# Performance work log

Measured on AMD Instinct MI355X. Metric: run time of the kernel, lower is better.

Reference implementation:

```python
import jax, jax.numpy as jnp
import numpy as np

NUM_VOCAB = 50000
EMBED_DIM = 128
SENT_SIZE = 50
MAX_HOPS = 3
BATCH = 128
MEM_SIZE = 200


def position_encoding(sentence_size, embedding_dim):
    # vectorized version of the original double loop
    i = np.arange(1, embedding_dim + 1, dtype=np.float32)[:, None]  # [D,1]
    j = np.arange(1, sentence_size + 1, dtype=np.float32)[None, :]  # [1,S]
    enc = (i - (embedding_dim + 1) / 2.0) * (j - (sentence_size + 1) / 2.0)
    enc = 1.0 + 4.0 * enc / embedding_dim / sentence_size
    enc[:, -1] = 1.0
    return np.transpose(enc).astype(np.float32)  # [S,D]


def setup_inputs() -> dict:
    key = jax.random.key(0)
    k1, k2, k3, k4, k5 = jax.random.split(key, 5)
    story = jax.random.randint(k1, (BATCH, MEM_SIZE, SENT_SIZE), 0, NUM_VOCAB, dtype=jnp.int64)
    query = jax.random.randint(k2, (BATCH, SENT_SIZE), 0, NUM_VOCAB, dtype=jnp.int64)
    # max_hops+1 embedding tables, N(0, 0.1), padding_idx=0 row zeroed
    C = 0.1 * jax.random.normal(k3, (MAX_HOPS + 1, NUM_VOCAB, EMBED_DIM), dtype=jnp.float32)
    C = C.at[:, 0, :].set(0.0)
    # T_k linear layer (PyTorch default uniform init bound)
    bound = 1.0 / np.sqrt(EMBED_DIM)
    T_w = jax.random.uniform(k4, (EMBED_DIM, EMBED_DIM), jnp.float32, -bound, bound)
    T_b = jax.random.uniform(k5, (EMBED_DIM,), jnp.float32, -bound, bound)
    return {"story": story, "query": query, "C": C, "T_w": T_w, "T_b": T_b}


def reference(story, query, C, T_w, T_b):
    enc = jnp.asarray(position_encoding(SENT_SIZE, EMBED_DIM))  # [S,D]
    # u0: position-encoded sum of query embedding
    q_emb = C[0][query]  # [B,S,D]
    u = jnp.einsum('bsd,sd->bd', q_emb, enc)
    for hop in range(MAX_HOPS):
        emb_A = C[hop][story]          # [B,M,S,D]
        m_A = jnp.einsum('bmsd,sd->bmd', emb_A, enc)
        prob = jax.nn.softmax(jnp.einsum('bmd,bd->bm', m_A, u), axis=-1)
        emb_C = C[hop + 1][story]      # [B,M,S,D]
        m_C = jnp.einsum('bmsd,sd->bmd', emb_C, enc)
        o_k = jnp.einsum('bmd,bm->bd', m_C, prob)
        t_k = jax.nn.sigmoid(u @ T_w.T + T_b)
        u = (1.0 - t_k) * u + o_k * t_k
    a_hat = u @ C[MAX_HOPS].T  # [B,V]
    return a_hat
```

## Files before the change

### kernel.cpp

```cpp
#include <hip/hip_runtime.h>
#include <cstdint>
#include <cstddef>

#define NV 50000
#define ED 128
#define SS 50
#define NB 128
#define NM 200
#define BMD (NB*NM*ED)
#define NCH 32
#define CHD 1563

typedef _Float16 f16x8 __attribute__((ext_vector_type(8)));
typedef _Float16 f16x4 __attribute__((ext_vector_type(4)));
typedef float    f32x4 __attribute__((ext_vector_type(4)));

__global__ __launch_bounds__(256) void story_embed_k(
    const int* __restrict__ story, const float* __restrict__ C,
    float* __restrict__ Mt) {
  const int wave = threadIdx.x >> 6;
  const int lane = threadIdx.x & 63;
  const int bm0 = blockIdx.x * 16;
  const int sl = (lane < SS) ? lane : (SS - 1);

  int idxg[4], cidg[4];
#pragma unroll
  for (int gg = 0; gg < 4; ++gg) {
    const int bm = bm0 + wave + 4 * gg;
    idxg[gg] = story[(size_t)bm * SS + sl];
    cidg[gg] = (lane < SS) ? (idxg[gg] / CHD) : -1;
  }
  const float a0 = ((float)(2*lane + 1) - 64.5f) * 6.25e-4f;
  const float a1 = ((float)(2*lane + 2) - 64.5f) * 6.25e-4f;
  float2 acc[4][4];
#pragma unroll
  for (int gg = 0; gg < 4; ++gg)
#pragma unroll
    for (int k = 0; k < 4; ++k) acc[gg][k] = make_float2(0.f, 0.f);

  for (int c = 0; c < NCH; ++c) {
#pragma unroll
    for (int gg = 0; gg < 4; ++gg) {
      unsigned long long mask = __ballot(cidg[gg] == c);
      while (mask) {
        const int s = __builtin_ctzll(mask);
        mask &= mask - 1;
        const int row = __shfl(idxg[gg], s);
        float e0, e1;
        if (s == SS - 1) { e0 = 1.0f; e1 = 1.0f; }
        else {
          float js = (float)(s + 1) - 25.5f;
          e0 = fmaf(a0, js, 1.0f);
          e1 = fmaf(a1, js, 1.0f);
        }
        const float* base = C + (size_t)row * ED + 2 * lane;
#pragma unroll
        for (int k = 0; k < 4; ++k) {
          float2 cv = *(const float2*)(base + (size_t)k * NV * ED);
          acc[gg][k].x = fmaf(e0, cv.x, acc[gg][k].x);
          acc[gg][k].y = fmaf(e1, cv.y, acc[gg][k].y);
        }
      }
    }
    __syncthreads();
  }

#pragma unroll
  for (int gg = 0; gg < 4; ++gg) {
    const int bm = bm0 + wave + 4 * gg;
#pragma unroll
    for (int k = 0; k < 4; ++k)
      *(float2*)(Mt + (size_t)k * BMD + (size_t)bm * ED + 2 * lane) = acc[gg][k];
  }
}

__global__ __launch_bounds__(512, 2) void hops_k(
    const int* __restrict__ query, const float* __restrict__ C,
    const float* __restrict__ Tw, const float* __restrict__ Tb,
    const float* __restrict__ Mt, float* __restrict__ U) {
  const int b = blockIdx.x;
  const int tid = threadIdx.x;
  const int d = tid & 127;
  const int p = tid >> 7;
  const int wave = tid >> 6, lane = tid & 63;
  __shared__ float tile[NM * ED];
  __shared__ float u[ED];
  __shared__ float part[512];
  __shared__ float sc[NM];
  __shared__ float o[ED];

  {
    const float4* s4 = (const float4*)(Mt + (size_t)b * NM * ED);
    float4* t4 = (float4*)tile;
    float4 st[13];
#pragma unroll
    for (int j = 0; j < 13; ++j) {
      int i = tid + 512 * j;
      st[j] = (i < NM * ED / 4) ? s4[i] : make_float4(0.f, 0.f, 0.f, 0.f);
    }
#pragma unroll
    for (int j = 0; j < 13; ++j) {
      int i = tid + 512 * j;
      if (i < NM * ED / 4) t4[i] = st[j];
    }
  }

  {
    const float ad = ((float)(d + 1) - 64.5f) * 6.25e-4f;
    int rows[13];
#pragma unroll
    for (int j = 0; j < 13; ++j) {
      int s = p + 4 * j;
      rows[j] = query[b * SS + (s < SS ? s : 0)];
    }
    float cv[13];
#pragma unroll
    for (int j = 0; j < 13; ++j)
      cv[j] = C[(size_t)rows[j] * ED + d];
    float accv = 0.f;
#pragma unroll
    for (int j = 0; j < 13; ++j) {
      int s = p + 4 * j;
      float e;
      if (s >= SS) e = 0.f;
      else if (s == SS - 1) e = 1.0f;
      else e = fmaf(ad, (float)(s + 1) - 25.5f, 1.0f);
      accv = fmaf(e, cv[j], accv);
    }
    part[tid] = accv;
  }
  __syncthreads();
  if (tid < ED)
    u[tid] = part[tid] + part[tid + 128] + part[tid + 256] + part[tid + 384];
  __syncthreads();

  for (int hop = 0; hop < 3; ++hop) {
    const float* Tn = Mt + (size_t)(hop + 1) * BMD + (size_t)b * NM * ED;
    float pf[50];
#pragma unroll
    for (int j = 0; j < 50; ++j)
      pf[j] = Tn[(size_t)(p + 4 * j) * ED + d];

    {
      float u0v = u[2 * lane], u1v = u[2 * lane + 1];
      for (int m = wave; m < NM; m += 16) {
        const int m2 = m + 8;
        const bool has2 = (m2 < NM);
        float2 r0 = *(const float2*)&tile[m * ED + 2 * lane];
        float pa = r0.x * u0v + r0.y * u1v;
        float pb = 0.f;
        if (has2) {
          float2 r1 = *(const float2*)&tile[m2 * ED + 2 * lane];
          pb = r1.x * u0v + r1.y * u1v;
        }
#pragma unroll
        for (int off = 32; off; off >>= 1) {
          pa += __shfl_xor(pa, off);
          pb += __shfl_xor(pb, off);
        }
        if (lane == 0) {
          sc[m] = pa;
          if (has2) sc[m2] = pb;
        }
      }
    }
    __syncthreads();

    float v = (tid < NM) ? sc[tid] : -1e30f;
    {
      float t = v;
#pragma unroll
      for (int off = 32; off; off >>= 1) t = fmaxf(t, __shfl_xor(t, off));
      if (lane == 0) part[wave] = t;
    }
    __syncthreads();
    float mx = part[0];
#pragma unroll
    for (int w = 1; w < 8; ++w) mx = fmaxf(mx, part[w]);
    float ev = 0.f;
    if (tid < NM) { ev = __expf(v - mx); sc[tid] = ev; }
    {
      float t = ev;
#pragma unroll
      for (int off = 32; off; off >>= 1) t += __shfl_xor(t, off);
      if (lane == 0) part[8 + wave] = t;
    }
    __syncthreads();
    float tot = part[8];
#pragma unroll
    for (int w = 9; w < 16; ++w) tot += part[w];
    const float inv = 1.0f / tot;
    __syncthreads();

    {
      float oacc = 0.f;
#pragma unroll
      for (int j = 0; j < 50; ++j)
        oacc = fmaf(sc[p + 4 * j], pf[j], oacc);
      part[tid] = oacc;
    }
    if (hop < 2) {
#pragma unroll
      for (int j = 0; j < 50; ++j)
        tile[(p + 4 * j) * ED + d] = pf[j];
    }
    __syncthreads();
    if (tid < ED)
      o[tid] = (part[tid] + part[tid + 128] + part[tid + 256] + part[tid + 384])
               * inv;
    __syncthreads();

    {
      const float4* twr = (const float4*)(Tw + (size_t)d * ED + p * 32);
      float4 tw4[8];
#pragma unroll
      for (int j = 0; j < 8; ++j) tw4[j] = twr[j];
      float tacc = 0.f;
#pragma unroll
      for (int j = 0; j < 8; ++j) {
        tacc = fmaf(u[p * 32 + 4 * j + 0], tw4[j].x, tacc);
        tacc = fmaf(u[p * 32 + 4 * j + 1], tw4[j].y, tacc);
        tacc = fmaf(u[p * 32 + 4 * j + 2], tw4[j].z, tacc);
        tacc = fmaf(u[p * 32 + 4 * j + 3], tw4[j].w, tacc);
      }
      part[tid] = tacc;
    }
    __syncthreads();
    if (tid < ED) {
      float dot = part[tid] + part[tid + 128] + part[tid + 256] + part[tid + 384]
                  + Tb[tid];
      float tk = 1.0f / (1.0f + __expf(-dot));
      u[tid] = (1.0f - tk) * u[tid] + o[tid] * tk;
    }
    __syncthreads();
  }
  if (tid < ED) U[(size_t)b * ED + tid] = u[tid];
}

__global__ __launch_bounds__(256) void cvt_c3_k(
    const float* __restrict__ src, _Float16* __restrict__ dst) {
  const int i = blockIdx.x * 256 + threadIdx.x;
  const float4* s4 = (const float4*)src;
  float4 f0 = s4[2 * i];
  float4 f1 = s4[2 * i + 1];
  f16x8 h;
  h[0] = (_Float16)f0.x; h[1] = (_Float16)f0.y;
  h[2] = (_Float16)f0.z; h[3] = (_Float16)f0.w;
  h[4] = (_Float16)f1.x; h[5] = (_Float16)f1.y;
  h[6] = (_Float16)f1.z; h[7] = (_Float16)f1.w;
  *(f16x8*)(dst + (size_t)8 * i) = h;
}

__global__ __launch_bounds__(256) void out_mm_mfma_k(
    const float* __restrict__ U, const _Float16* __restrict__ C3h,
    float* __restrict__ out) {
  __shared__ _Float16 Ub[ED * 136];
  const int tid = threadIdx.x;

  {
    const float4* u4 = (const float4*)U;
#pragma unroll
    for (int j = 0; j < 16; ++j) {
      int i = tid + 256 * j;
      float4 f = u4[i];
      int row = i >> 5;
      int col = (i & 31) * 4;
      f16x4 h;
      h[0] = (_Float16)f.x; h[1] = (_Float16)f.y;
      h[2] = (_Float16)f.z; h[3] = (_Float16)f.w;
      *(f16x4*)&Ub[row * 136 + col] = h;
    }
  }
  __syncthreads();

  const int wave = tid >> 6, lane = tid & 63;
  const int n = lane & 15, q = lane >> 4;
  const int v = blockIdx.x * 64 + wave * 16 + n;
  const bool vok = (v < NV);

  f32x4 acc[8];
#pragma unroll
  for (int mt = 0; mt < 8; ++mt) acc[mt] = (f32x4){0.f, 0.f, 0.f, 0.f};

#pragma unroll
  for (int kt = 0; kt < 4; ++kt) {
    f16x8 bfrag = {};
    if (vok) bfrag = *(const f16x8*)(C3h + (size_t)v * ED + kt * 32 + q * 8);
#pragma unroll
    for (int mt = 0; mt < 8; ++mt) {
      f16x8 afrag = *(const f16x8*)&Ub[(mt * 16 + n) * 136 + kt * 32 + q * 8];
      acc[mt] = __builtin_amdgcn_mfma_f32_16x16x32_f16(afrag, bfrag, acc[mt],
                                                       0, 0, 0);
    }
  }

  if (vok) {
#pragma unroll
    for (int mt = 0; mt < 8; ++mt)
#pragma unroll
      for (int i = 0; i < 4; ++i)
        out[(size_t)(mt * 16 + q * 4 + i) * NV + v] = acc[mt][i];
  }
}

extern "C" void kernel_launch(void* const* d_in, const int* in_sizes, int n_in,
                              void* d_out, int out_size, void* d_ws, size_t ws_size,
                              hipStream_t stream) {
  const int*   story = (const int*)d_in[0];
  const int*   query = (const int*)d_in[1];
  const float* C     = (const float*)d_in[2];
  const float* Tw    = (const float*)d_in[3];
  const float* Tb    = (const float*)d_in[4];
  float* out = (float*)d_out;

  float* wsf = (float*)d_ws;
  float*     Mt  = wsf;
  float*     U   = wsf + (size_t)4 * BMD;
  _Float16*  C3h = (_Float16*)(wsf + (size_t)4 * BMD + NB * ED);

  hipLaunchKernelGGL(story_embed_k, dim3(NB * NM / 16), dim3(256), 0, stream,
                     story, C, Mt);
  hipLaunchKernelGGL(hops_k, dim3(NB), dim3(512), 0, stream,
                     query, C, Tw, Tb, Mt, U);
  hipLaunchKernelGGL(cvt_c3_k, dim3(NV * ED / 8 / 256), dim3(256), 0, stream,
                     C + (size_t)3 * NV * ED, C3h);
  hipLaunchKernelGGL(out_mm_mfma_k, dim3((NV + 63) / 64), dim3(256), 0, stream,
                     U, C3h, out);
}
```

Before: 409.8 us.

## Fuse C3 fp16 conversion into story embed and stream hop memories from global

The fp32-to-fp16 conversion of the last embedding table moves into the story embedding kernel, so one launch goes away and the conversion can overlap with the gather work. The hops kernel drops its 100KB shared-memory tile and the 50-register prefetch. It now reads the memory rows for scoring and the output rows for the weighted sum directly from global memory (likely L2-resident), in batches of ten. This reduces LDS and register pressure and the staging copies, at the cost of more global or L2 reads per hop.

Measured after the change: 414.6 us. About the same (+1.2%).

```diff
diff --git a/kernel.cpp b/kernel.cpp
--- a/kernel.cpp
+++ b/kernel.cpp
@@ -17,7 +17,23 @@
 
 __global__ __launch_bounds__(256) void story_embed_k(
     const int* __restrict__ story, const float* __restrict__ C,
-    float* __restrict__ Mt) {
+    float* __restrict__ Mt, _Float16* __restrict__ C3h) {
+  {
+    const float* C3 = C + (size_t)3 * NV * ED;
+    const int base4 = blockIdx.x * 1024;
+#pragma unroll
+    for (int r = 0; r < 4; ++r) {
+      int i4 = base4 + r * 256 + threadIdx.x;
+      if (i4 < NV * ED / 4) {
+        float4 f = ((const float4*)C3)[i4];
+        f16x4 h;
+        h[0] = (_Float16)f.x; h[1] = (_Float16)f.y;
+        h[2] = (_Float16)f.z; h[3] = (_Float16)f.w;
+        *(f16x4*)(C3h + (size_t)4 * i4) = h;
+      }
+    }
+  }
+
   const int wave = threadIdx.x >> 6;
   const int lane = threadIdx.x & 63;
   const int bm0 = blockIdx.x * 16;
@@ -74,7 +90,7 @@
   }
 }
 
-__global__ __launch_bounds__(512, 2) void hops_k(
+__global__ __launch_bounds__(512) void hops_k(
     const int* __restrict__ query, const float* __restrict__ C,
     const float* __restrict__ Tw, const float* __restrict__ Tb,
     const float* __restrict__ Mt, float* __restrict__ U) {
@@ -83,27 +99,10 @@
   const int d = tid & 127;
   const int p = tid >> 7;
   const int wave = tid >> 6, lane = tid & 63;
-  __shared__ float tile[NM * ED];
   __shared__ float u[ED];
   __shared__ float part[512];
   __shared__ float sc[NM];
   __shared__ float o[ED];
-
-  {
-    const float4* s4 = (const float4*)(Mt + (size_t)b * NM * ED);
-    float4* t4 = (float4*)tile;
-    float4 st[13];
-#pragma unroll
-    for (int j = 0; j < 13; ++j) {
-      int i = tid + 512 * j;
-      st[j] = (i < NM * ED / 4) ? s4[i] : make_float4(0.f, 0.f, 0.f, 0.f);
-    }
-#pragma unroll
-    for (int j = 0; j < 13; ++j) {
-      int i = tid + 512 * j;
-      if (i < NM * ED / 4) t4[i] = st[j];
-    }
-  }
 
   {
     const float ad = ((float)(d + 1) - 64.5f) * 6.25e-4f;
@@ -135,32 +134,32 @@
   __syncthreads();
 
   for (int hop = 0; hop < 3; ++hop) {
-    const float* Tn = Mt + (size_t)(hop + 1) * BMD + (size_t)b * NM * ED;
-    float pf[50];
-#pragma unroll
-    for (int j = 0; j < 50; ++j)
-      pf[j] = Tn[(size_t)(p + 4 * j) * ED + d];
+    const float* MA = Mt + (size_t)hop * BMD + (size_t)b * NM * ED;
+    const float* MC = MA + BMD;
 
     {
       float u0v = u[2 * lane], u1v = u[2 * lane + 1];
-      for (int m = wave; m < NM; m += 16) {
-        const int m2 = m + 8;
-        const bool has2 = (m2 < NM);
-        float2 r0 = *(const float2*)&tile[m * ED + 2 * lane];
-        float pa = r0.x * u0v + r0.y * u1v;
-        float pb = 0.f;
-        if (has2) {
-          float2 r1 = *(const float2*)&tile[m2 * ED + 2 * lane];
-          pb = r1.x * u0v + r1.y * u1v;
+      for (int m = wave; m < NM; m += 32) {
+        float pa[4] = {0.f, 0.f, 0.f, 0.f};
+#pragma unroll
+        for (int t = 0; t < 4; ++t) {
+          int mm = m + 8 * t;
+          if (mm < NM) {
+            float2 r = *(const float2*)(MA + (size_t)mm * ED + 2 * lane);
+            pa[t] = r.x * u0v + r.y * u1v;
+          }
         }
 #pragma unroll
         for (int off = 32; off; off >>= 1) {
-          pa += __shfl_xor(pa, off);
-          pb += __shfl_xor(pb, off);
+#pragma unroll
+          for (int t = 0; t < 4; ++t) pa[t] += __shfl_xor(pa[t], off);
         }
         if (lane == 0) {
-          sc[m] = pa;
-          if (has2) sc[m2] = pb;
+#pragma unroll
+          for (int t = 0; t < 4; ++t) {
+            int mm = m + 8 * t;
+            if (mm < NM) sc[mm] = pa[t];
+          }
         }
       }
     }
@@ -195,14 +194,16 @@
     {
       float oacc = 0.f;
 #pragma unroll
-      for (int j = 0; j < 50; ++j)
-        oacc = fmaf(sc[p + 4 * j], pf[j], oacc);
+      for (int jb = 0; jb < 5; ++jb) {
+        float vbuf[10];
+#pragma unroll
+        for (int j = 0; j < 10; ++j)
+          vbuf[j] = MC[(size_t)(p + 4 * (jb * 10 + j)) * ED + d];
+#pragma unroll
+        for (int j = 0; j < 10; ++j)
+          oacc = fmaf(sc[p + 4 * (jb * 10 + j)], vbuf[j], oacc);
+      }
       part[tid] = oacc;
-    }
-    if (hop < 2) {
-#pragma unroll
-      for (int j = 0; j < 50; ++j)
-        tile[(p + 4 * j) * ED + d] = pf[j];
     }
     __syncthreads();
     if (tid < ED)
@@ -235,20 +236,6 @@
     __syncthreads();
   }
   if (tid < ED) U[(size_t)b * ED + tid] = u[tid];
-}
-
-__global__ __launch_bounds__(256) void cvt_c3_k(
-    const float* __restrict__ src, _Float16* __restrict__ dst) {
-  const int i = blockIdx.x * 256 + threadIdx.x;
-  const float4* s4 = (const float4*)src;
-  float4 f0 = s4[2 * i];
-  float4 f1 = s4[2 * i + 1];
-  f16x8 h;
-  h[0] = (_Float16)f0.x; h[1] = (_Float16)f0.y;
-  h[2] = (_Float16)f0.z; h[3] = (_Float16)f0.w;
-  h[4] = (_Float16)f1.x; h[5] = (_Float16)f1.y;
-  h[6] = (_Float16)f1.z; h[7] = (_Float16)f1.w;
-  *(f16x8*)(dst + (size_t)8 * i) = h;
 }
 
 __global__ __launch_bounds__(256) void out_mm_mfma_k(
@@ -319,11 +306,9 @@
   _Float16*  C3h = (_Float16*)(wsf + (size_t)4 * BMD + NB * ED);
 
   hipLaunchKernelGGL(story_embed_k, dim3(NB * NM / 16), dim3(256), 0, stream,
-                     story, C, Mt);
+                     story, C, Mt, C3h);
   hipLaunchKernelGGL(hops_k, dim3(NB), dim3(512), 0, stream,
                      query, C, Tw, Tb, Mt, U);
-  hipLaunchKernelGGL(cvt_c3_k, dim3(NV * ED / 8 / 256), dim3(256), 0, stream,
-                     C + (size_t)3 * NV * ED, C3h);
   hipLaunchKernelGGL(out_mm_mfma_k, dim3((NV + 63) / 64), dim3(256), 0, stream,
                      U, C3h, out);
 }
```
